# Kernel tuning notes

Measured on AMD Instinct MI355X. Metric: run time of the kernel, lower is better.

The kernel has to match this reference:

```python
import jax, jax.numpy as jnp
import numpy as np

N_NODES = 100000
N_EDGES = 1000000
N_LABEL = 200000
D_IN = 128
D_HID = 128


def setup_inputs() -> dict:
    key = jax.random.key(0)
    k1, k2, k3, k4, k5 = jax.random.split(key, 5)
    node_feature = jax.random.normal(k1, (N_NODES, D_IN), dtype=jnp.float32)
    edge_index = jax.random.randint(k2, (2, N_EDGES), 0, N_NODES, dtype=jnp.int64)
    edge_label_index = jax.random.randint(k3, (2, N_LABEL), 0, N_NODES, dtype=jnp.int64)
    W1 = jax.random.normal(k4, (D_IN, D_HID), dtype=jnp.float32) * (1.0 / np.sqrt(D_IN))
    b1 = jnp.zeros((D_HID,), dtype=jnp.float32)
    W2 = jax.random.normal(k5, (D_HID, D_HID), dtype=jnp.float32) * (1.0 / np.sqrt(D_HID))
    b2 = jnp.zeros((D_HID,), dtype=jnp.float32)
    return {"node_feature": node_feature, "edge_index": edge_index,
            "edge_label_index": edge_label_index,
            "W1": W1, "b1": b1, "W2": W2, "b2": b2}


def reference(node_feature, edge_index, edge_label_index, W1, b1, W2, b2):
    N = node_feature.shape[0]
    # GCN normalization with added self-loops (PyG GCNConv default)
    loop = jnp.arange(N, dtype=edge_index.dtype)
    src = jnp.concatenate([edge_index[0], loop])  # [E+N]
    dst = jnp.concatenate([edge_index[1], loop])  # [E+N]
    deg = jax.ops.segment_sum(jnp.ones_like(dst, dtype=node_feature.dtype), dst, N)
    dinv = jnp.where(deg > 0, jax.lax.rsqrt(deg), 0.0)
    norm = dinv[src] * dinv[dst]  # [E+N]

    def gcn_conv(x, W, b):
        h = x @ W                              # [N, d] transform first (d small)
        msg = h[src] * norm[:, None]           # gather + scale over edges
        return jax.ops.segment_sum(msg, dst, N) + b  # scatter-add to targets

    # eval mode: dropout(p=0.2) is identity
    x = jax.nn.relu(gcn_conv(node_feature, W1, b1))
    x = gcn_conv(x, W2, b2)

    # edge scoring: gather both endpoints, elementwise mul, sum over features
    nodes_first = x[edge_label_index[0]]
    nodes_second = x[edge_label_index[1]]
    pred = jnp.sum(nodes_first * nodes_second, axis=-1)  # [N_LABEL]
    return pred
```

## Files before the change

kernel.cpp:

```cpp
#include <hip/hip_runtime.h>
#include <hip/hip_bf16.h>


#define N_NODES 100000
#define N_EDGES 1000000
#define N_LABEL 200000
#define D_FEAT 128
#define BM 128

#define NB 782
#define BCAP 2048
#define P1_EPT 16
#define P1_BLOCKS 245
#define G_GEMM 782

typedef short bf16x8 __attribute__((ext_vector_type(8)));
typedef float f32x4 __attribute__((ext_vector_type(4)));

__device__ inline unsigned int f2bf(float x) {
    unsigned int u = __float_as_uint(x);
    return (u + 0x7FFFu + ((u >> 16) & 1u)) >> 16;
}
__device__ inline unsigned int bf16pack(float a, float b) {
    return f2bf(a) | (f2bf(b) << 16);
}
__device__ inline float bflo(unsigned int u) { return __uint_as_float(u << 16); }
__device__ inline float bfhi(unsigned int u) { return __uint_as_float(u & 0xFFFF0000u); }

__global__ __launch_bounds__(256) void pass1_bucket_w2bf(
    const int* __restrict__ src, const int* __restrict__ dst,
    int* __restrict__ gcur, unsigned int* __restrict__ temp,
    const float* __restrict__ W1, const float* __restrict__ W2,
    unsigned short* __restrict__ Wt1, unsigned short* __restrict__ Wt2) {
    int b = blockIdx.x, t = threadIdx.x;
    if (b >= P1_BLOCKS) {
        int i = (b - P1_BLOCKS) * 256 + t;
        const float* W = (i < 16384) ? W1 : W2;
        unsigned short* Wt = (i < 16384) ? Wt1 : Wt2;
        int j = i & 16383;
        int n = j >> 7, k = j & 127;
        Wt[j] = (unsigned short)f2bf(W[(size_t)k * 128 + n]);
        return;
    }
    __shared__ int hist[NB], base[NB];
    for (int i = t; i < NB; i += 256) hist[i] = 0;
    __syncthreads();

    int se[P1_EPT], de[P1_EPT], rk[P1_EPT];
    int e0 = b * (P1_EPT * 256) + t;
#pragma unroll
    for (int j = 0; j < P1_EPT; ++j) {
        int e = e0 + j * 256;
        if (e < N_EDGES) {
            se[j] = src[e];
            de[j] = dst[e];
            rk[j] = atomicAdd(&hist[de[j] >> 7], 1);
        }
    }
    __syncthreads();
    for (int i = t; i < NB; i += 256) {
        int h = hist[i];
        base[i] = h ? atomicAdd(&gcur[i], h) : 0;
    }
    __syncthreads();
#pragma unroll
    for (int j = 0; j < P1_EPT; ++j) {
        int e = e0 + j * 256;
        if (e < N_EDGES) {
            int k = de[j] >> 7;
            int pos = base[k] + rk[j];
            if (pos < BCAP)
                temp[(size_t)k * BCAP + pos] =
                    (unsigned int)(((de[j] & 127) << 17) | se[j]);
        }
    }
}

template <bool BF16_IN>
__device__ __forceinline__ void gemm_body(const void* __restrict__ Xv,
                                          const unsigned short* __restrict__ Wt,
                                          unsigned int* __restrict__ Y,
                                          int nrows, int bid, short* Ws) {
    int t = threadIdx.x;
#pragma unroll
    for (int i = 0; i < 8; ++i) {
        int c = i * 256 + t;
        int n = c >> 4, q = c & 15;
        uint4 v = *(const uint4*)&Wt[(size_t)n * 128 + q * 8];
        *(uint4*)&Ws[n * 128 + ((q ^ (n & 15)) << 3)] = v;
    }
    __syncthreads();

    int wv = t >> 6;
    int lane = t & 63, l16 = lane & 15, quad = lane >> 4;
    int rbase = bid * BM + wv * 32;

    f32x4 acc[2][8];
#pragma unroll
    for (int rt = 0; rt < 2; ++rt)
#pragma unroll
        for (int nt = 0; nt < 8; ++nt) acc[rt][nt] = (f32x4){0.f, 0.f, 0.f, 0.f};

#pragma unroll
    for (int kb = 0; kb < 4; ++kb) {
        bf16x8 af[2];
#pragma unroll
        for (int rt = 0; rt < 2; ++rt) {
            int row = rbase + rt * 16 + l16;
            if (row > nrows - 1) row = nrows - 1;
            if constexpr (BF16_IN) {
                const unsigned int* Xb = (const unsigned int*)Xv;
                af[rt] = *(const bf16x8*)&Xb[(size_t)row * 64 + kb * 16 + quad * 4];
            } else {
                const float* X = (const float*)Xv;
                float4 fa = ((const float4*)X)[(size_t)row * 32 + kb * 8 + quad * 2];
                float4 fb = ((const float4*)X)[(size_t)row * 32 + kb * 8 + quad * 2 + 1];
                union { uint4 u; bf16x8 v; } cv;
                cv.u.x = bf16pack(fa.x, fa.y);
                cv.u.y = bf16pack(fa.z, fa.w);
                cv.u.z = bf16pack(fb.x, fb.y);
                cv.u.w = bf16pack(fb.z, fb.w);
                af[rt] = cv.v;
            }
        }
        bf16x8 bfr[8];
#pragma unroll
        for (int nt = 0; nt < 8; ++nt) {
            int n = nt * 16 + l16;
            bfr[nt] = *(const bf16x8*)&Ws[n * 128 + (((kb * 4 + quad) ^ l16) << 3)];
        }
#pragma unroll
        for (int rt = 0; rt < 2; ++rt)
#pragma unroll
            for (int nt = 0; nt < 8; ++nt)
                acc[rt][nt] = __builtin_amdgcn_mfma_f32_16x16x32_bf16(
                    af[rt], bfr[nt], acc[rt][nt], 0, 0, 0);
    }

    short* Ys = (short*)Y;
#pragma unroll
    for (int rt = 0; rt < 2; ++rt)
#pragma unroll
        for (int reg = 0; reg < 4; ++reg) {
            int row = rbase + rt * 16 + quad * 4 + reg;
            if (row < nrows) {
#pragma unroll
                for (int nt = 0; nt < 8; ++nt)
                    Ys[(size_t)row * 128 + nt * 16 + l16] = (short)f2bf(acc[rt][nt][reg]);
            }
        }
}

__global__ __launch_bounds__(256) void gemm128_mfma_bf16(const unsigned int* __restrict__ Xb,
                                                         const unsigned short* __restrict__ Wt,
                                                         unsigned int* __restrict__ Y,
                                                         int nrows) {
    __shared__ __align__(16) short Ws[128 * 128];
    gemm_body<true>(Xb, Wt, Y, nrows, blockIdx.x, Ws);
}

__global__ __launch_bounds__(256) void fused_gemm1_pass2(
    const float* __restrict__ feat, const unsigned short* __restrict__ wt1,
    unsigned int* __restrict__ Hb, const int* __restrict__ gcur,
    const unsigned int* __restrict__ temp, int* __restrict__ row_ptr,
    float* __restrict__ dinv, int* __restrict__ packed) {
    __shared__ __align__(16) short Ws[128 * 128];
    int b = blockIdx.x, t = threadIdx.x;
    if (b < G_GEMM) {
        gemm_body<false>(feat, wt1, Hb, N_NODES, b, Ws);
        return;
    }
    int k = b - G_GEMM;
    unsigned int* ed = (unsigned int*)Ws;
    int* hist = (int*)(ed + BCAP);
    int* rp = hist + 128;
    int* cur = rp + 128;
    int* sc = cur + 128;
    int* red = sc + 128;

    int part = 0;
    for (int j = t; j < NB; j += 256)
        if (j < k) part += gcur[j];
    red[t] = part;
    __syncthreads();
    for (int off = 128; off > 0; off >>= 1) {
        if (t < off) red[t] += red[t + off];
        __syncthreads();
    }
    int gbase = red[0];
    int nk = gcur[k];
    if (nk > BCAP) nk = BCAP;

    if (t < 128) { hist[t] = 0; cur[t] = 0; }
    __syncthreads();
    for (int i = t; i < nk; i += 256) {
        unsigned int v = temp[(size_t)k * BCAP + i];
        ed[i] = v;
        atomicAdd(&hist[v >> 17], 1);
    }
    __syncthreads();

    if (t < 128) sc[t] = hist[t];
    __syncthreads();
    for (int off = 1; off < 128; off <<= 1) {
        int a = (t < 128 && t >= off) ? sc[t - off] : 0;
        __syncthreads();
        if (t < 128) sc[t] += a;
        __syncthreads();
    }
    if (t < 128) {
        rp[t] = sc[t] - hist[t];
        int n = k * 128 + t;
        if (n < N_NODES) {
            row_ptr[n] = gbase + rp[t];
            dinv[n] = rsqrtf((float)(hist[t] + 1));
        }
    }
    if (k == NB - 1 && t == 0) row_ptr[N_NODES] = N_EDGES;
    __syncthreads();

    for (int i = t; i < nk; i += 256) {
        unsigned int v = ed[i];
        int dl = v >> 17;
        int r = atomicAdd(&cur[dl], 1);
        packed[gbase + rp[dl] + r] = (int)(v & 0x1FFFF);
    }
}

template <bool RELU>
__global__ __launch_bounds__(256) void aggregate(const unsigned int* __restrict__ Hb,
                                                 const int* __restrict__ packed,
                                                 const int* __restrict__ row_ptr,
                                                 const float* __restrict__ dinv,
                                                 const float* __restrict__ bias,
                                                 unsigned int* __restrict__ Xb) {
    int v0 = blockIdx.x * 8 + (threadIdx.x >> 6) * 2;
    int v1 = v0 + 1;
    int lane = threadIdx.x & 63;
    if (v0 >= N_NODES) return;
    bool h1 = (v1 < N_NODES);

    int st0 = row_ptr[v0], en0 = row_ptr[v0 + 1];
    int st1 = h1 ? row_ptr[v1] : 0, en1 = h1 ? row_ptr[v1 + 1] : 0;
    float dv0 = dinv[v0];
    float dv1 = h1 ? dinv[v1] : 0.f;

    unsigned int su0 = Hb[(size_t)v0 * 64 + lane];
    float a0 = dv0 * bflo(su0), a1 = dv0 * bfhi(su0);
    unsigned int su1 = h1 ? Hb[(size_t)v1 * 64 + lane] : 0u;
    float b0 = dv1 * bflo(su1), b1 = dv1 * bfhi(su1);

    int p = 0;
    if (lane < 32) {
        if (st0 + lane < en0) p = packed[st0 + lane];
    } else {
        if (st1 + lane - 32 < en1) p = packed[st1 + lane - 32];
    }

    for (int c0 = st0, c1 = st1; c0 < en0 || c1 < en1; c0 += 32, c1 += 32) {
        int n0 = en0 - c0; n0 = n0 < 0 ? 0 : (n0 > 32 ? 32 : n0);
        int n1 = en1 - c1; n1 = n1 < 0 ? 0 : (n1 > 32 ? 32 : n1);
        bool act = (lane < 32) ? (lane < n0) : (lane - 32 < n1);
        float dld = dinv[p];
        float d = act ? dld : 0.f;

        int nmax = n0 > n1 ? n0 : n1;
        int pn = 0;
        bool pref = false;
        for (int j = 0; j < nmax; j += 8) {
            int sA[8], sB[8];
#pragma unroll
            for (int q = 0; q < 8; ++q) {
                sA[q] = __shfl(p, j + q);
                sB[q] = __shfl(p, 32 + j + q);
            }
            unsigned int uA[8], uB[8];
#pragma unroll
            for (int q = 0; q < 8; ++q) {
                uA[q] = Hb[(size_t)sA[q] * 64 + lane];
                uB[q] = Hb[(size_t)sB[q] * 64 + lane];
            }
            if (!pref) {
                pref = true;
                if (lane < 32) {
                    if (c0 + 32 + lane < en0) pn = packed[c0 + 32 + lane];
                } else {
                    if (c1 + lane < en1) pn = packed[c1 + lane];
                }
            }
            float dA[8], dB[8];
#pragma unroll
            for (int q = 0; q < 8; ++q) {
                dA[q] = __shfl(d, j + q);
                dB[q] = __shfl(d, 32 + j + q);
            }
#pragma unroll
            for (int q = 0; q < 8; ++q) {
                a0 = fmaf(dA[q], bflo(uA[q]), a0);
                a1 = fmaf(dA[q], bfhi(uA[q]), a1);
                b0 = fmaf(dB[q], bflo(uB[q]), b0);
                b1 = fmaf(dB[q], bfhi(uB[q]), b1);
            }
        }
        p = pn;
    }

    float2 bb = ((const float2*)bias)[lane];
    a0 = fmaf(a0, dv0, bb.x);
    a1 = fmaf(a1, dv0, bb.y);
    b0 = fmaf(b0, dv1, bb.x);
    b1 = fmaf(b1, dv1, bb.y);
    if (RELU) {
        a0 = fmaxf(a0, 0.f);
        a1 = fmaxf(a1, 0.f);
        b0 = fmaxf(b0, 0.f);
        b1 = fmaxf(b1, 0.f);
    }
    Xb[(size_t)v0 * 64 + lane] = bf16pack(a0, a1);
    if (h1) Xb[(size_t)v1 * 64 + lane] = bf16pack(b0, b1);
}

__global__ __launch_bounds__(256) void score_kernel(const int* __restrict__ ea,
                                                    const int* __restrict__ eb,
                                                    const unsigned int* __restrict__ Xb,
                                                    float* __restrict__ out) {
    int wbase = (blockIdx.x * 4 + (threadIdx.x >> 6)) * 4;
    int lane = threadIdx.x & 63;
    if (wbase >= N_LABEL) return;
    int ne = N_LABEL - wbase;
    if (ne > 4) ne = 4;

    unsigned int ua[4], ub[4];
#pragma unroll
    for (int e = 0; e < 4; ++e)
        if (e < ne) {
            int ia = ea[wbase + e], ib = eb[wbase + e];
            ua[e] = Xb[(size_t)ia * 64 + lane];
            ub[e] = Xb[(size_t)ib * 64 + lane];
        }
#pragma unroll
    for (int e = 0; e < 4; ++e)
        if (e < ne) {
            float p = bflo(ua[e]) * bflo(ub[e]) + bfhi(ua[e]) * bfhi(ub[e]);
#pragma unroll
            for (int off = 32; off > 0; off >>= 1) p += __shfl_down(p, off);
            if (lane == 0) out[wbase + e] = p;
        }
}

extern "C" void kernel_launch(void* const* d_in, const int* in_sizes, int n_in,
                              void* d_out, int out_size, void* d_ws, size_t ws_size,
                              hipStream_t stream) {
    const float* feat = (const float*)d_in[0];
    const int* ei = (const int*)d_in[1];
    const int* eli = (const int*)d_in[2];
    const float* W1 = (const float*)d_in[3];
    const float* b1 = (const float*)d_in[4];
    const float* W2 = (const float*)d_in[5];
    const float* b2 = (const float*)d_in[6];
    float* out = (float*)d_out;

    const int* src = ei;
    const int* dst = ei + N_EDGES;
    const int* la = eli;
    const int* lb = eli + N_LABEL;

    int* gcur = (int*)d_ws;
    int* row_ptr = gcur + 1024;
    float* dinv = (float*)(row_ptr + N_NODES + 4);
    unsigned short* wt1 = (unsigned short*)(dinv + N_NODES);
    unsigned short* wt2 = wt1 + 16384;
    int* packed = (int*)(wt2 + 16384);
    unsigned int* Hb = (unsigned int*)(packed + N_EDGES);
    unsigned int* Xb = Hb + (size_t)N_NODES * 64;
    unsigned int* temp = Xb;

    const int TB = 256;
    int gGemm = (N_NODES + BM - 1) / BM;
    int gAgg = (N_NODES + 7) / 8;
    int gScore = (N_LABEL + 15) / 16;

    hipMemsetAsync(gcur, 0, NB * sizeof(int), stream);

    pass1_bucket_w2bf<<<P1_BLOCKS + 128, TB, 0, stream>>>(src, dst, gcur, temp,
                                                          W1, W2, wt1, wt2);

    fused_gemm1_pass2<<<G_GEMM + NB, TB, 0, stream>>>(feat, wt1, Hb, gcur, temp,
                                                      row_ptr, dinv, packed);

    aggregate<true><<<gAgg, TB, 0, stream>>>(Hb, packed, row_ptr, dinv, b1, Xb);

    gemm128_mfma_bf16<<<gGemm, TB, 0, stream>>>(Xb, wt2, Hb, N_NODES);
    aggregate<false><<<gAgg, TB, 0, stream>>>(Hb, packed, row_ptr, dinv, b2, Xb);

    score_kernel<<<gScore, TB, 0, stream>>>(la, lb, Xb, out);
}
```

Measured before the change: 282.4 us.

## Overlap edge bucketing with first GEMM and split sorting into its own kernel

Edge bucketing (pass1) now runs as extra blocks of the layer-1 GEMM kernel, where bucket sorting (pass2) used to sit. Pass2 becomes a standalone kernel with its own small shared-memory footprint. Zeroing the bucket counters moves from a memset call into the weight-conversion kernel, so the weights are converted before the GEMM starts. The aim is to hide pass1's atomic-heavy work behind the GEMM and give pass2 better occupancy, at the cost of pass2 now running serially after the GEMM, and pass1 blocks inheriting the GEMM's 32 KB LDS allocation.

Measured after the change: 279.4 us. No clear change (-1.1%).

```diff
diff --git a/kernel.cpp b/kernel.cpp
--- a/kernel.cpp
+++ b/kernel.cpp
@@ -13,6 +13,7 @@
 #define P1_EPT 16
 #define P1_BLOCKS 245
 #define G_GEMM 782
+#define G_CONV 128
 
 typedef short bf16x8 __attribute__((ext_vector_type(8)));
 typedef float f32x4 __attribute__((ext_vector_type(4)));
@@ -27,53 +28,21 @@
 __device__ inline float bflo(unsigned int u) { return __uint_as_float(u << 16); }
 __device__ inline float bfhi(unsigned int u) { return __uint_as_float(u & 0xFFFF0000u); }
 
-__global__ __launch_bounds__(256) void pass1_bucket_w2bf(
-    const int* __restrict__ src, const int* __restrict__ dst,
-    int* __restrict__ gcur, unsigned int* __restrict__ temp,
+__global__ __launch_bounds__(256) void w2bf_zero(
     const float* __restrict__ W1, const float* __restrict__ W2,
-    unsigned short* __restrict__ Wt1, unsigned short* __restrict__ Wt2) {
+    unsigned short* __restrict__ Wt1, unsigned short* __restrict__ Wt2,
+    int* __restrict__ gcur) {
     int b = blockIdx.x, t = threadIdx.x;
-    if (b >= P1_BLOCKS) {
-        int i = (b - P1_BLOCKS) * 256 + t;
-        const float* W = (i < 16384) ? W1 : W2;
-        unsigned short* Wt = (i < 16384) ? Wt1 : Wt2;
-        int j = i & 16383;
-        int n = j >> 7, k = j & 127;
-        Wt[j] = (unsigned short)f2bf(W[(size_t)k * 128 + n]);
+    if (b == G_CONV) {
+        ((int4*)gcur)[t] = make_int4(0, 0, 0, 0);
         return;
     }
-    __shared__ int hist[NB], base[NB];
-    for (int i = t; i < NB; i += 256) hist[i] = 0;
-    __syncthreads();
-
-    int se[P1_EPT], de[P1_EPT], rk[P1_EPT];
-    int e0 = b * (P1_EPT * 256) + t;
-#pragma unroll
-    for (int j = 0; j < P1_EPT; ++j) {
-        int e = e0 + j * 256;
-        if (e < N_EDGES) {
-            se[j] = src[e];
-            de[j] = dst[e];
-            rk[j] = atomicAdd(&hist[de[j] >> 7], 1);
-        }
-    }
-    __syncthreads();
-    for (int i = t; i < NB; i += 256) {
-        int h = hist[i];
-        base[i] = h ? atomicAdd(&gcur[i], h) : 0;
-    }
-    __syncthreads();
-#pragma unroll
-    for (int j = 0; j < P1_EPT; ++j) {
-        int e = e0 + j * 256;
-        if (e < N_EDGES) {
-            int k = de[j] >> 7;
-            int pos = base[k] + rk[j];
-            if (pos < BCAP)
-                temp[(size_t)k * BCAP + pos] =
-                    (unsigned int)(((de[j] & 127) << 17) | se[j]);
-        }
-    }
+    int i = b * 256 + t;
+    const float* W = (i < 16384) ? W1 : W2;
+    unsigned short* Wt = (i < 16384) ? Wt1 : Wt2;
+    int j = i & 16383;
+    int n = j >> 7, k = j & 127;
+    Wt[j] = (unsigned short)f2bf(W[(size_t)k * 128 + n]);
 }
 
 template <bool BF16_IN>
@@ -159,24 +128,61 @@
     gemm_body<true>(Xb, Wt, Y, nrows, blockIdx.x, Ws);
 }
 
-__global__ __launch_bounds__(256) void fused_gemm1_pass2(
+__global__ __launch_bounds__(256) void fused_gemm1_pass1(
     const float* __restrict__ feat, const unsigned short* __restrict__ wt1,
-    unsigned int* __restrict__ Hb, const int* __restrict__ gcur,
-    const unsigned int* __restrict__ temp, int* __restrict__ row_ptr,
-    float* __restrict__ dinv, int* __restrict__ packed) {
+    unsigned int* __restrict__ Hb,
+    const int* __restrict__ src, const int* __restrict__ dst,
+    int* __restrict__ gcur, unsigned int* __restrict__ temp) {
     __shared__ __align__(16) short Ws[128 * 128];
     int b = blockIdx.x, t = threadIdx.x;
     if (b < G_GEMM) {
         gemm_body<false>(feat, wt1, Hb, N_NODES, b, Ws);
         return;
     }
-    int k = b - G_GEMM;
-    unsigned int* ed = (unsigned int*)Ws;
-    int* hist = (int*)(ed + BCAP);
-    int* rp = hist + 128;
-    int* cur = rp + 128;
-    int* sc = cur + 128;
-    int* red = sc + 128;
+    b -= G_GEMM;
+    int* hist = (int*)Ws;
+    int* base = hist + NB;
+    for (int i = t; i < NB; i += 256) hist[i] = 0;
+    __syncthreads();
+
+    int se[P1_EPT], de[P1_EPT], rk[P1_EPT];
+    int e0 = b * (P1_EPT * 256) + t;
+#pragma unroll
+    for (int j = 0; j < P1_EPT; ++j) {
+        int e = e0 + j * 256;
+        if (e < N_EDGES) {
+            se[j] = src[e];
+            de[j] = dst[e];
+            rk[j] = atomicAdd(&hist[de[j] >> 7], 1);
+        }
+    }
+    __syncthreads();
+    for (int i = t; i < NB; i += 256) {
+        int h = hist[i];
+        base[i] = h ? atomicAdd(&gcur[i], h) : 0;
+    }
+    __syncthreads();
+#pragma unroll
+    for (int j = 0; j < P1_EPT; ++j) {
+        int e = e0 + j * 256;
+        if (e < N_EDGES) {
+            int k = de[j] >> 7;
+            int pos = base[k] + rk[j];
+            if (pos < BCAP)
+                temp[(size_t)k * BCAP + pos] =
+                    (unsigned int)(((de[j] & 127) << 17) | se[j]);
+        }
+    }
+}
+
+__global__ __launch_bounds__(256) void pass2_sort(
+    const int* __restrict__ gcur, const unsigned int* __restrict__ temp,
+    int* __restrict__ row_ptr, float* __restrict__ dinv,
+    int* __restrict__ packed) {
+    int k = blockIdx.x, t = threadIdx.x;
+    __shared__ unsigned int ed[BCAP];
+    __shared__ int hist[128], rp[128], cur[128], sc[128];
+    __shared__ int red[256];
 
     int part = 0;
     for (int j = t; j < NB; j += 256)
@@ -380,13 +386,12 @@
     int gAgg = (N_NODES + 7) / 8;
     int gScore = (N_LABEL + 15) / 16;
 
-    hipMemsetAsync(gcur, 0, NB * sizeof(int), stream);
-
-    pass1_bucket_w2bf<<<P1_BLOCKS + 128, TB, 0, stream>>>(src, dst, gcur, temp,
-                                                          W1, W2, wt1, wt2);
-
-    fused_gemm1_pass2<<<G_GEMM + NB, TB, 0, stream>>>(feat, wt1, Hb, gcur, temp,
-                                                      row_ptr, dinv, packed);
+    w2bf_zero<<<G_CONV + 1, TB, 0, stream>>>(W1, W2, wt1, wt2, gcur);
+
+    fused_gemm1_pass1<<<G_GEMM + P1_BLOCKS, TB, 0, stream>>>(
+        feat, wt1, Hb, src, dst, gcur, temp);
+
+    pass2_sort<<<NB, TB, 0, stream>>>(gcur, temp, row_ptr, dinv, packed);
 
     aggregate<true><<<gAgg, TB, 0, stream>>>(Hb, packed, row_ptr, dinv, b1, Xb);
 
```
